# Kernel optimization log

Hardware: AMD Instinct MI355X
Metric: run time of the kernel (lower is better)

## Reference

```python
import jax, jax.numpy as jnp
import numpy as np

ALPHA = 5.0   # surrogate sharpness (cfg.alpha)
C = 0.4       # surrogate scale (cfg.c)
Q = 120.0     # adaptation current scale (cfg.q)
THR = 1.0     # spike threshold

@jax.custom_vjp
def spike(u_thr):
    # Heaviside forward; SLAYER-style surrogate gradient injection backward.
    return (u_thr > 0).astype(u_thr.dtype)

def _spike_fwd(u_thr):
    return spike(u_thr), u_thr

def _spike_bwd(u_thr, g):
    return (g * C * jnp.exp(-ALPHA * jnp.abs(u_thr)),)

spike.defvjp(_spike_fwd, _spike_bwd)


def setup_inputs() -> dict:
    key = jax.random.key(0)
    ks = jax.random.split(key, 8)
    B, T, I, N = 32, 2000, 256, 512
    x = jax.random.normal(ks[0], (B, T, I), dtype=jnp.float32)
    lim = 1.0 / np.sqrt(I)
    weight = jax.random.uniform(ks[1], (N, I), jnp.float32, -lim, lim)
    bias = jnp.zeros((N,), jnp.float32)
    # orthogonal init for recurrent weights (torch.nn.init.orthogonal_)
    g = jax.random.normal(ks[2], (N, N), jnp.float32)
    q_, r_ = jnp.linalg.qr(g)
    recurrent = q_ * jnp.sign(jnp.diagonal(r_))[None, :]
    # membrane / adaptation decays: exp(-dt/tau), tau uniform in cfg ranges
    tau_u = jax.random.uniform(ks[3], (N,), jnp.float32, 5.0, 25.0)
    tau_w = jax.random.uniform(ks[4], (N,), jnp.float32, 60.0, 300.0)
    decay_u = jnp.exp(-1.0 / tau_u)
    decay_w = jnp.exp(-1.0 / tau_w)
    a = jax.random.uniform(ks[5], (N,), jnp.float32, 0.0, 1.0)
    b = jax.random.uniform(ks[6], (N,), jnp.float32, 0.0, 2.0)
    return dict(x=x, weight=weight, bias=bias, recurrent=recurrent,
                decay_u=decay_u, decay_w=decay_w, a=a, b=b)


def reference(x, weight, bias, recurrent, decay_u, decay_w, a, b):
    # soma current for all timesteps at once: [B, T, N]
    cur = jnp.einsum('bti,ni->btn', x, weight) + bias
    B, T, N = cur.shape
    u0 = jnp.zeros((B, N), cur.dtype)  # u0 param is zero-init (train_u0=False)
    z0 = jnp.zeros((B, N), cur.dtype)
    w0 = jnp.zeros((B, N), cur.dtype)

    def step(carry, c_t):
        u_tm1, z_tm1, w_tm1 = carry
        c_t = c_t + z_tm1 @ recurrent.T               # recurrent input
        u = decay_u * u_tm1 + (1.0 - decay_u) * (c_t - w_tm1)
        z = spike(u - THR)
        zd = jax.lax.stop_gradient(z)
        u = u * (1.0 - zd)                            # reset to u_rest = 0
        w = decay_w * w_tm1 + (1.0 - decay_w) * (a * u_tm1 + b * z_tm1) * Q
        return (u, z, w), z

    cur_t = jnp.swapaxes(cur, 0, 1)                   # [T, B, N]
    _, zs = jax.lax.scan(step, (u0, z0, w0), cur_t)
    return jnp.swapaxes(zs, 0, 1)                     # [B, T, N]
```

## Files before the change

kernel.cpp:

```cpp
#include <hip/hip_runtime.h>
#include <cstdint>
#include <cstddef>

#define NB 32
#define NT 2000
#define NI 256
#define NN 512
#define M_TOT (NB * NT)
#define DS 8

typedef float f32x4 __attribute__((ext_vector_type(4)));

__global__ void transpose_R(const float* __restrict__ R, float* __restrict__ Rt) {
    int idx = blockIdx.x * blockDim.x + threadIdx.x;
    if (idx >= NN * NN) return;
    int j = idx >> 9;
    int n = idx & (NN - 1);
    Rt[idx] = R[n * NN + j];
}

#define GBM 128
#define GBN 128
#define GBK 16
__global__ __launch_bounds__(256) void gemm_xw(const float* __restrict__ A,
                                               const float* __restrict__ Wt,
                                               const float* __restrict__ bias,
                                               float* __restrict__ C) {
    __shared__ float As[GBK][GBM];
    __shared__ float Bs[GBK][GBN];
    const int tid = threadIdx.x;
    const int bm = blockIdx.x * GBM;
    const int bn = blockIdx.y * GBN;
    const int tx = tid & 15, ty = tid >> 4;
    const int lrow = tid >> 1;
    const int lk = (tid & 1) * 8;
    float acc[8][8] = {};
    const float* Arow = A + (size_t)(bm + lrow) * NI + lk;
    const float* Brow = Wt + (size_t)(bn + lrow) * NI + lk;
    for (int k0 = 0; k0 < NI; k0 += GBK) {
        float4 a0 = *(const float4*)(Arow + k0);
        float4 a1 = *(const float4*)(Arow + k0 + 4);
        float4 b0 = *(const float4*)(Brow + k0);
        float4 b1 = *(const float4*)(Brow + k0 + 4);
        __syncthreads();
        As[lk + 0][lrow] = a0.x; As[lk + 1][lrow] = a0.y;
        As[lk + 2][lrow] = a0.z; As[lk + 3][lrow] = a0.w;
        As[lk + 4][lrow] = a1.x; As[lk + 5][lrow] = a1.y;
        As[lk + 6][lrow] = a1.z; As[lk + 7][lrow] = a1.w;
        Bs[lk + 0][lrow] = b0.x; Bs[lk + 1][lrow] = b0.y;
        Bs[lk + 2][lrow] = b0.z; Bs[lk + 3][lrow] = b0.w;
        Bs[lk + 4][lrow] = b1.x; Bs[lk + 5][lrow] = b1.y;
        Bs[lk + 6][lrow] = b1.z; Bs[lk + 7][lrow] = b1.w;
        __syncthreads();
        #pragma unroll
        for (int k = 0; k < GBK; ++k) {
            float4 av0 = *(const float4*)&As[k][ty * 8];
            float4 av1 = *(const float4*)&As[k][ty * 8 + 4];
            float4 bv0 = *(const float4*)&Bs[k][tx * 8];
            float4 bv1 = *(const float4*)&Bs[k][tx * 8 + 4];
            float a_[8] = {av0.x, av0.y, av0.z, av0.w, av1.x, av1.y, av1.z, av1.w};
            float b_[8] = {bv0.x, bv0.y, bv0.z, bv0.w, bv1.x, bv1.y, bv1.z, bv1.w};
            #pragma unroll
            for (int i = 0; i < 8; ++i)
                #pragma unroll
                for (int j = 0; j < 8; ++j)
                    acc[i][j] += a_[i] * b_[j];
        }
    }
    #pragma unroll
    for (int i = 0; i < 8; ++i) {
        const int row = bm + ty * 8 + i;
        #pragma unroll
        for (int j = 0; j < 8; ++j) {
            const int col = bn + tx * 8 + j;
            C[(size_t)row * NN + col] = acc[i][j] + bias[col];
        }
    }
}


#define UPD(C_, R_, DU_, ODU_, DW_, ODW_, A_, B_, U_, W_, Z_) do {               \
    float cc_   = __fadd_rn((C_), (R_));                                         \
    float unew_ = __fadd_rn(__fmul_rn((DU_), (U_)),                              \
                            __fmul_rn((ODU_), __fsub_rn(cc_, (W_))));            \
    float zn_   = (__fsub_rn(unew_, 1.0f) > 0.0f) ? 1.0f : 0.0f;                 \
    float s_    = __fadd_rn(__fmul_rn((A_), (U_)), __fmul_rn((B_), (Z_)));       \
    float wnew_ = __fadd_rn(__fmul_rn((DW_), (W_)),                              \
                            __fmul_rn(__fmul_rn((ODW_), s_), 120.0f));           \
    (U_) = __fmul_rn(unew_, __fsub_rn(1.0f, zn_));                               \
    (W_) = wnew_;                                                                \
    (Z_) = zn_;                                                                  \
} while (0)

#define HLOAD(DA, DB, PTR)                                                       \
    asm volatile("global_load_dwordx4 %0, %2, off\n\t"                           \
                 "global_load_dwordx4 %1, %2, off offset:16"                     \
                 : "=&v"(DA), "=&v"(DB) : "v"(PTR))

__global__ __launch_bounds__(128, 1) void scan_pc(const float* __restrict__ cur,
        const float* __restrict__ Rm,
        const float* __restrict__ du_g, const float* __restrict__ dw_g,
        const float* __restrict__ a_g, const float* __restrict__ b_g,
        float* __restrict__ out) {
    __shared__ float curlds[DS][NN];
    const int tid = threadIdx.x;
    const int lane = tid & 63;
    const int b = blockIdx.x;
    const float* curb = cur + (size_t)b * NT * NN;

    if (tid >= 64) {
        const int off = lane << 3;
        float4 q0a, q0b, q1a, q1b, q2a, q2b, q3a, q3b;
        #define PLOAD(QA, QB, STEP) do {                                          \
            const float* p_ = curb + (size_t)(STEP) * NN + off;                   \
            QA = *(const float4*)p_; QB = *(const float4*)(p_ + 4);               \
        } while (0)
        #define PSTORE(QA, QB, STEP) do {                                         \
            int sl_ = (STEP) & (DS - 1);                                          \
            *(float4*)&curlds[sl_][off] = QA;                                     \
            *(float4*)&curlds[sl_][off + 4] = QB;                                 \
        } while (0)
        PLOAD(q0a, q0b, 0); PLOAD(q1a, q1b, 1); PLOAD(q2a, q2b, 2); PLOAD(q3a, q3b, 3);
        PSTORE(q0a, q0b, 0); PSTORE(q1a, q1b, 1); PSTORE(q2a, q2b, 2);
        PLOAD(q0a, q0b, 4); PLOAD(q1a, q1b, 5); PLOAD(q2a, q2b, 6);
        #define PSTEP(QA, QB, T) do {                                             \
            int ws_ = (T) + 3; if (ws_ > NT - 1) ws_ = NT - 1;                    \
            int ls_ = (T) + 7; if (ls_ > NT - 1) ls_ = NT - 1;                    \
            PSTORE(QA, QB, ws_);                                                  \
            PLOAD(QA, QB, ls_);                                                   \
            asm volatile("s_waitcnt lgkmcnt(0)" ::: "memory");                    \
            __builtin_amdgcn_s_barrier();                                         \
        } while (0)
        for (int t = 0; t < NT; t += 4) {
            PSTEP(q3a, q3b, t + 0);
            PSTEP(q0a, q0b, t + 1);
            PSTEP(q1a, q1b, t + 2);
            PSTEP(q2a, q2b, t + 3);
        }
        #undef PSTEP
        #undef PSTORE
        #undef PLOAD
    } else {
        const int n0 = lane << 3;

        const float4 du0 = *(const float4*)(du_g + n0);
        const float4 du1 = *(const float4*)(du_g + n0 + 4);
        const float4 dw0 = *(const float4*)(dw_g + n0);
        const float4 dw1 = *(const float4*)(dw_g + n0 + 4);
        const float4 an0 = *(const float4*)(a_g + n0);
        const float4 an1 = *(const float4*)(a_g + n0 + 4);
        const float4 bn0 = *(const float4*)(b_g + n0);
        const float4 bn1 = *(const float4*)(b_g + n0 + 4);
        const float4 odu0 = {1.0f - du0.x, 1.0f - du0.y, 1.0f - du0.z, 1.0f - du0.w};
        const float4 odu1 = {1.0f - du1.x, 1.0f - du1.y, 1.0f - du1.z, 1.0f - du1.w};
        const float4 odw0 = {1.0f - dw0.x, 1.0f - dw0.y, 1.0f - dw0.z, 1.0f - dw0.w};
        const float4 odw1 = {1.0f - dw1.x, 1.0f - dw1.y, 1.0f - dw1.z, 1.0f - dw1.w};

        float4 u0 = {0,0,0,0}, u1 = {0,0,0,0};
        float4 w0 = {0,0,0,0}, w1 = {0,0,0,0};
        float4 z0 = {0,0,0,0}, z1 = {0,0,0,0};
        unsigned long long m0=0,m1=0,m2=0,m3=0,m4=0,m5=0,m6=0,m7=0;

        float* outp = out + (size_t)b * NT * NN + n0;

        for (int t = 0; t < NT; ++t) {
            __builtin_amdgcn_s_barrier();
            __builtin_amdgcn_sched_barrier(0);
            asm volatile("" ::: "memory");
            const int slot = t & (DS - 1);
            float4 c0 = *(const float4*)&curlds[slot][n0];
            float4 c1 = *(const float4*)&curlds[slot][n0 + 4];

            float4 r0 = {0,0,0,0}, r1 = {0,0,0,0};
            if (m0 | m1 | m2 | m3 | m4 | m5 | m6 | m7) {
                #define HEADJ(MM, E) ((MM) ? ((__builtin_ctzll(MM) << 3) + (E)) : 0)
                const float* hp0 = Rm + ((size_t)HEADJ(m0, 0) << 9) + n0;
                const float* hp1 = Rm + ((size_t)HEADJ(m1, 1) << 9) + n0;
                const float* hp2 = Rm + ((size_t)HEADJ(m2, 2) << 9) + n0;
                const float* hp3 = Rm + ((size_t)HEADJ(m3, 3) << 9) + n0;
                const float* hp4 = Rm + ((size_t)HEADJ(m4, 4) << 9) + n0;
                const float* hp5 = Rm + ((size_t)HEADJ(m5, 5) << 9) + n0;
                const float* hp6 = Rm + ((size_t)HEADJ(m6, 6) << 9) + n0;
                const float* hp7 = Rm + ((size_t)HEADJ(m7, 7) << 9) + n0;
                #undef HEADJ
                f32x4 h0a, h0b, h1a, h1b, h2a, h2b, h3a, h3b;
                f32x4 h4a, h4b, h5a, h5b, h6a, h6b, h7a, h7b;
                HLOAD(h0a, h0b, hp0);
                HLOAD(h1a, h1b, hp1);
                HLOAD(h2a, h2b, hp2);
                HLOAD(h3a, h3b, hp3);
                HLOAD(h4a, h4b, hp4);
                HLOAD(h5a, h5b, hp5);
                HLOAD(h6a, h6b, hp6);
                HLOAD(h7a, h7b, hp7);
                asm volatile("s_waitcnt vmcnt(0)" ::: "memory");
                __builtin_amdgcn_sched_barrier(0);

                #define ACC(QA, QB) do {                                          \
                    r0.x = __fadd_rn(r0.x, (QA).x); r0.y = __fadd_rn(r0.y, (QA).y);\
                    r0.z = __fadd_rn(r0.z, (QA).z); r0.w = __fadd_rn(r0.w, (QA).w);\
                    r1.x = __fadd_rn(r1.x, (QB).x); r1.y = __fadd_rn(r1.y, (QB).y);\
                    r1.z = __fadd_rn(r1.z, (QB).z); r1.w = __fadd_rn(r1.w, (QB).w);\
                } while (0)
                #define PROC(MM, E, HA, HB) do {                                  \
                    if (MM) {                                                     \
                        ACC(HA, HB);                                              \
                        unsigned long long g_ = (MM) & ((MM) - 1);                \
                        while (g_) {                                              \
                            int l_ = __builtin_ctzll(g_); g_ &= g_ - 1;           \
                            int j_ = (l_ << 3) + (E);                             \
                            const float* rp_ = Rm + ((size_t)j_ << 9) + n0;       \
                            float4 q0_ = *(const float4*)rp_;                     \
                            float4 q1_ = *(const float4*)(rp_ + 4);               \
                            ACC(q0_, q1_);                                        \
                        }                                                         \
                    }                                                             \
                } while (0)
                PROC(m0, 0, h0a, h0b); PROC(m1, 1, h1a, h1b);
                PROC(m2, 2, h2a, h2b); PROC(m3, 3, h3a, h3b);
                PROC(m4, 4, h4a, h4b); PROC(m5, 5, h5a, h5b);
                PROC(m6, 6, h6a, h6b); PROC(m7, 7, h7a, h7b);
                #undef PROC
                #undef ACC
            }

            UPD(c0.x, r0.x, du0.x, odu0.x, dw0.x, odw0.x, an0.x, bn0.x, u0.x, w0.x, z0.x);
            UPD(c0.y, r0.y, du0.y, odu0.y, dw0.y, odw0.y, an0.y, bn0.y, u0.y, w0.y, z0.y);
            UPD(c0.z, r0.z, du0.z, odu0.z, dw0.z, odw0.z, an0.z, bn0.z, u0.z, w0.z, z0.z);
            UPD(c0.w, r0.w, du0.w, odu0.w, dw0.w, odw0.w, an0.w, bn0.w, u0.w, w0.w, z0.w);
            UPD(c1.x, r1.x, du1.x, odu1.x, dw1.x, odw1.x, an1.x, bn1.x, u1.x, w1.x, z1.x);
            UPD(c1.y, r1.y, du1.y, odu1.y, dw1.y, odw1.y, an1.y, bn1.y, u1.y, w1.y, z1.y);
            UPD(c1.z, r1.z, du1.z, odu1.z, dw1.z, odw1.z, an1.z, bn1.z, u1.z, w1.z, z1.z);
            UPD(c1.w, r1.w, du1.w, odu1.w, dw1.w, odw1.w, an1.w, bn1.w, u1.w, w1.w, z1.w);

            m0 = __ballot(z0.x > 0.5f);
            m1 = __ballot(z0.y > 0.5f);
            m2 = __ballot(z0.z > 0.5f);
            m3 = __ballot(z0.w > 0.5f);
            m4 = __ballot(z1.x > 0.5f);
            m5 = __ballot(z1.y > 0.5f);
            m6 = __ballot(z1.z > 0.5f);
            m7 = __ballot(z1.w > 0.5f);

            *(float4*)outp = z0;
            *(float4*)(outp + 4) = z1;
            outp += NN;
        }
    }
}

__global__ __launch_bounds__(64) void scan_fallback(const float* __restrict__ cur,
        const float* __restrict__ Rm,
        const float* __restrict__ du_g, const float* __restrict__ dw_g,
        const float* __restrict__ a_g, const float* __restrict__ b_g,
        float* __restrict__ out) {
    const int lane = threadIdx.x & 63;
    const int b = blockIdx.x;
    const int n0 = lane << 3;
    const float4 du0 = *(const float4*)(du_g + n0);
    const float4 du1 = *(const float4*)(du_g + n0 + 4);
    const float4 dw0 = *(const float4*)(dw_g + n0);
    const float4 dw1 = *(const float4*)(dw_g + n0 + 4);
    const float4 an0 = *(const float4*)(a_g + n0);
    const float4 an1 = *(const float4*)(a_g + n0 + 4);
    const float4 bn0 = *(const float4*)(b_g + n0);
    const float4 bn1 = *(const float4*)(b_g + n0 + 4);
    const float4 odu0 = {1.0f - du0.x, 1.0f - du0.y, 1.0f - du0.z, 1.0f - du0.w};
    const float4 odu1 = {1.0f - du1.x, 1.0f - du1.y, 1.0f - du1.z, 1.0f - du1.w};
    const float4 odw0 = {1.0f - dw0.x, 1.0f - dw0.y, 1.0f - dw0.z, 1.0f - dw0.w};
    const float4 odw1 = {1.0f - dw1.x, 1.0f - dw1.y, 1.0f - dw1.z, 1.0f - dw1.w};
    float4 u0 = {0,0,0,0}, u1 = {0,0,0,0};
    float4 w0 = {0,0,0,0}, w1 = {0,0,0,0};
    float4 z0 = {0,0,0,0}, z1 = {0,0,0,0};
    unsigned long long m0=0,m1=0,m2=0,m3=0,m4=0,m5=0,m6=0,m7=0;
    const float* curp = cur + (size_t)b * NT * NN + n0;
    float* outp = out + (size_t)b * NT * NN + n0;
    for (int t = 0; t < NT; ++t) {
        float4 c0 = *(const float4*)(curp);
        float4 c1 = *(const float4*)(curp + 4);
        curp += NN;
        float4 r0 = {0,0,0,0}, r1 = {0,0,0,0};
        #define GATHER(MM, E) do {                                                \
            unsigned long long g_ = (MM);                                         \
            while (g_) {                                                          \
                int l_ = __builtin_ctzll(g_); g_ &= g_ - 1;                       \
                int j_ = (l_ << 3) + (E);                                         \
                float q0x_ = Rm[(size_t)(n0 + 0) * NN + j_];                      \
                float q0y_ = Rm[(size_t)(n0 + 1) * NN + j_];                      \
                float q0z_ = Rm[(size_t)(n0 + 2) * NN + j_];                      \
                float q0w_ = Rm[(size_t)(n0 + 3) * NN + j_];                      \
                float q1x_ = Rm[(size_t)(n0 + 4) * NN + j_];                      \
                float q1y_ = Rm[(size_t)(n0 + 5) * NN + j_];                      \
                float q1z_ = Rm[(size_t)(n0 + 6) * NN + j_];                      \
                float q1w_ = Rm[(size_t)(n0 + 7) * NN + j_];                      \
                r0.x = __fadd_rn(r0.x, q0x_); r0.y = __fadd_rn(r0.y, q0y_);       \
                r0.z = __fadd_rn(r0.z, q0z_); r0.w = __fadd_rn(r0.w, q0w_);       \
                r1.x = __fadd_rn(r1.x, q1x_); r1.y = __fadd_rn(r1.y, q1y_);       \
                r1.z = __fadd_rn(r1.z, q1z_); r1.w = __fadd_rn(r1.w, q1w_);       \
            }                                                                     \
        } while (0)
        GATHER(m0, 0); GATHER(m1, 1); GATHER(m2, 2); GATHER(m3, 3);
        GATHER(m4, 4); GATHER(m5, 5); GATHER(m6, 6); GATHER(m7, 7);
        #undef GATHER
        UPD(c0.x, r0.x, du0.x, odu0.x, dw0.x, odw0.x, an0.x, bn0.x, u0.x, w0.x, z0.x);
        UPD(c0.y, r0.y, du0.y, odu0.y, dw0.y, odw0.y, an0.y, bn0.y, u0.y, w0.y, z0.y);
        UPD(c0.z, r0.z, du0.z, odu0.z, dw0.z, odw0.z, an0.z, bn0.z, u0.z, w0.z, z0.z);
        UPD(c0.w, r0.w, du0.w, odu0.w, dw0.w, odw0.w, an0.w, bn0.w, u0.w, w0.w, z0.w);
        UPD(c1.x, r1.x, du1.x, odu1.x, dw1.x, odw1.x, an1.x, bn1.x, u1.x, w1.x, z1.x);
        UPD(c1.y, r1.y, du1.y, odu1.y, dw1.y, odw1.y, an1.y, bn1.y, u1.y, w1.y, z1.y);
        UPD(c1.z, r1.z, du1.z, odu1.z, dw1.z, odw1.z, an1.z, bn1.z, u1.z, w1.z, z1.z);
        UPD(c1.w, r1.w, du1.w, odu1.w, dw1.w, odw1.w, an1.w, bn1.w, u1.w, w1.w, z1.w);
        m0 = __ballot(z0.x > 0.5f);
        m1 = __ballot(z0.y > 0.5f);
        m2 = __ballot(z0.z > 0.5f);
        m3 = __ballot(z0.w > 0.5f);
        m4 = __ballot(z1.x > 0.5f);
        m5 = __ballot(z1.y > 0.5f);
        m6 = __ballot(z1.z > 0.5f);
        m7 = __ballot(z1.w > 0.5f);
        *(float4*)outp = z0;
        *(float4*)(outp + 4) = z1;
        outp += NN;
    }
}

extern "C" void kernel_launch(void* const* d_in, const int* in_sizes, int n_in,
                              void* d_out, int out_size, void* d_ws, size_t ws_size,
                              hipStream_t stream) {
    const float* x    = (const float*)d_in[0];
    const float* W    = (const float*)d_in[1];
    const float* bias = (const float*)d_in[2];
    const float* R    = (const float*)d_in[3];
    const float* du   = (const float*)d_in[4];
    const float* dw   = (const float*)d_in[5];
    const float* a    = (const float*)d_in[6];
    const float* b    = (const float*)d_in[7];
    float* out = (float*)d_out;

    const size_t curBytes = (size_t)M_TOT * NN * sizeof(float);
    const size_t rtBytes  = (size_t)NN * NN * sizeof(float);
    float* Rt  = nullptr;
    float* cur;
    if (ws_size >= rtBytes + curBytes) {
        Rt  = (float*)d_ws;
        cur = (float*)d_ws + (size_t)NN * NN;
    } else if (ws_size >= rtBytes) {
        Rt  = (float*)d_ws;
        cur = out;
    } else {
        cur = out;
    }

    if (Rt) {
        transpose_R<<<(NN * NN + 255) / 256, 256, 0, stream>>>(R, Rt);
    }
    dim3 ggrid(M_TOT / GBM, NN / GBN);
    gemm_xw<<<ggrid, 256, 0, stream>>>(x, W, bias, cur);
    if (Rt) {
        scan_pc<<<NB, 128, 0, stream>>>(cur, Rt, du, dw, a, b, out);
    } else {
        scan_fallback<<<NB, 64, 0, stream>>>(cur, R, du, dw, a, b, out);
    }
}
```

Baseline: 1.113 ms.

## Prefetch first two spike rows per mask right after ballot, split LDS layout

Moves the head recurrent-row loads from the start of the next step to right after the ballot, so they overlap the output stores and the barrier wait. It also loads the first two spiking rows per mask group instead of one. The LDS cur buffer is re-laid out into two halves of 256 floats with lane<<2 indexing, presumably to reduce bank conflicts on the float4 reads and writes. The cost is 64 extra VGPRs held across the loop, plus inline asm loads that stay outstanding across the barrier until vmcnt(0).

After: 1.230 ms. 10.5% more time.

```diff
diff --git a/kernel.cpp b/kernel.cpp
--- a/kernel.cpp
+++ b/kernel.cpp
@@ -102,7 +102,7 @@
         const float* __restrict__ du_g, const float* __restrict__ dw_g,
         const float* __restrict__ a_g, const float* __restrict__ b_g,
         float* __restrict__ out) {
-    __shared__ float curlds[DS][NN];
+    __shared__ float curlds[DS][2][256];
     const int tid = threadIdx.x;
     const int lane = tid & 63;
     const int b = blockIdx.x;
@@ -110,6 +110,7 @@
 
     if (tid >= 64) {
         const int off = lane << 3;
+        const int lo4 = lane << 2;
         float4 q0a, q0b, q1a, q1b, q2a, q2b, q3a, q3b;
         #define PLOAD(QA, QB, STEP) do {                                          \
             const float* p_ = curb + (size_t)(STEP) * NN + off;                   \
@@ -117,8 +118,8 @@
         } while (0)
         #define PSTORE(QA, QB, STEP) do {                                         \
             int sl_ = (STEP) & (DS - 1);                                          \
-            *(float4*)&curlds[sl_][off] = QA;                                     \
-            *(float4*)&curlds[sl_][off + 4] = QB;                                 \
+            *(float4*)&curlds[sl_][0][lo4] = QA;                                  \
+            *(float4*)&curlds[sl_][1][lo4] = QB;                                  \
         } while (0)
         PLOAD(q0a, q0b, 0); PLOAD(q1a, q1b, 1); PLOAD(q2a, q2b, 2); PLOAD(q3a, q3b, 3);
         PSTORE(q0a, q0b, 0); PSTORE(q1a, q1b, 1); PSTORE(q2a, q2b, 2);
@@ -142,6 +143,7 @@
         #undef PLOAD
     } else {
         const int n0 = lane << 3;
+        const int lo4 = lane << 2;
 
         const float4 du0 = *(const float4*)(du_g + n0);
         const float4 du1 = *(const float4*)(du_g + n0 + 4);
@@ -161,6 +163,9 @@
         float4 z0 = {0,0,0,0}, z1 = {0,0,0,0};
         unsigned long long m0=0,m1=0,m2=0,m3=0,m4=0,m5=0,m6=0,m7=0;
 
+        f32x4 h0a,h0b,h0c,h0d, h1a,h1b,h1c,h1d, h2a,h2b,h2c,h2d, h3a,h3b,h3c,h3d;
+        f32x4 h4a,h4b,h4c,h4d, h5a,h5b,h5c,h5d, h6a,h6b,h6c,h6d, h7a,h7b,h7c,h7d;
+
         float* outp = out + (size_t)b * NT * NN + n0;
 
         for (int t = 0; t < NT; ++t) {
@@ -168,31 +173,11 @@
             __builtin_amdgcn_sched_barrier(0);
             asm volatile("" ::: "memory");
             const int slot = t & (DS - 1);
-            float4 c0 = *(const float4*)&curlds[slot][n0];
-            float4 c1 = *(const float4*)&curlds[slot][n0 + 4];
+            float4 c0 = *(const float4*)&curlds[slot][0][lo4];
+            float4 c1 = *(const float4*)&curlds[slot][1][lo4];
 
             float4 r0 = {0,0,0,0}, r1 = {0,0,0,0};
             if (m0 | m1 | m2 | m3 | m4 | m5 | m6 | m7) {
-                #define HEADJ(MM, E) ((MM) ? ((__builtin_ctzll(MM) << 3) + (E)) : 0)
-                const float* hp0 = Rm + ((size_t)HEADJ(m0, 0) << 9) + n0;
-                const float* hp1 = Rm + ((size_t)HEADJ(m1, 1) << 9) + n0;
-                const float* hp2 = Rm + ((size_t)HEADJ(m2, 2) << 9) + n0;
-                const float* hp3 = Rm + ((size_t)HEADJ(m3, 3) << 9) + n0;
-                const float* hp4 = Rm + ((size_t)HEADJ(m4, 4) << 9) + n0;
-                const float* hp5 = Rm + ((size_t)HEADJ(m5, 5) << 9) + n0;
-                const float* hp6 = Rm + ((size_t)HEADJ(m6, 6) << 9) + n0;
-                const float* hp7 = Rm + ((size_t)HEADJ(m7, 7) << 9) + n0;
-                #undef HEADJ
-                f32x4 h0a, h0b, h1a, h1b, h2a, h2b, h3a, h3b;
-                f32x4 h4a, h4b, h5a, h5b, h6a, h6b, h7a, h7b;
-                HLOAD(h0a, h0b, hp0);
-                HLOAD(h1a, h1b, hp1);
-                HLOAD(h2a, h2b, hp2);
-                HLOAD(h3a, h3b, hp3);
-                HLOAD(h4a, h4b, hp4);
-                HLOAD(h5a, h5b, hp5);
-                HLOAD(h6a, h6b, hp6);
-                HLOAD(h7a, h7b, hp7);
                 asm volatile("s_waitcnt vmcnt(0)" ::: "memory");
                 __builtin_amdgcn_sched_barrier(0);
 
@@ -202,25 +187,33 @@
                     r1.x = __fadd_rn(r1.x, (QB).x); r1.y = __fadd_rn(r1.y, (QB).y);\
                     r1.z = __fadd_rn(r1.z, (QB).z); r1.w = __fadd_rn(r1.w, (QB).w);\
                 } while (0)
-                #define PROC(MM, E, HA, HB) do {                                  \
+                #define PROC2(MM, E, HA, HB, HC, HD) do {                         \
                     if (MM) {                                                     \
                         ACC(HA, HB);                                              \
                         unsigned long long g_ = (MM) & ((MM) - 1);                \
-                        while (g_) {                                              \
-                            int l_ = __builtin_ctzll(g_); g_ &= g_ - 1;           \
-                            int j_ = (l_ << 3) + (E);                             \
-                            const float* rp_ = Rm + ((size_t)j_ << 9) + n0;       \
-                            float4 q0_ = *(const float4*)rp_;                     \
-                            float4 q1_ = *(const float4*)(rp_ + 4);               \
-                            ACC(q0_, q1_);                                        \
+                        if (g_) {                                                 \
+                            ACC(HC, HD);                                          \
+                            g_ &= g_ - 1;                                         \
+                            while (g_) {     \
+                                int l_ = __builtin_ctzll(g_); g_ &= g_ - 1;       \
+                                int j_ = (l_ << 3) + (E);                         \
+                                const float* rp_ = Rm + ((size_t)j_ << 9) + n0;   \
+                                float4 q0_ = *(const float4*)rp_;                 \
+                                float4 q1_ = *(const float4*)(rp_ + 4);           \
+                                ACC(q0_, q1_);                                    \
+                            }                                                     \
                         }                                                         \
                     }                                                             \
                 } while (0)
-                PROC(m0, 0, h0a, h0b); PROC(m1, 1, h1a, h1b);
-                PROC(m2, 2, h2a, h2b); PROC(m3, 3, h3a, h3b);
-                PROC(m4, 4, h4a, h4b); PROC(m5, 5, h5a, h5b);
-                PROC(m6, 6, h6a, h6b); PROC(m7, 7, h7a, h7b);
-                #undef PROC
+                PROC2(m0, 0, h0a, h0b, h0c, h0d);
+                PROC2(m1, 1, h1a, h1b, h1c, h1d);
+                PROC2(m2, 2, h2a, h2b, h2c, h2d);
+                PROC2(m3, 3, h3a, h3b, h3c, h3d);
+                PROC2(m4, 4, h4a, h4b, h4c, h4d);
+                PROC2(m5, 5, h5a, h5b, h5c, h5d);
+                PROC2(m6, 6, h6a, h6b, h6c, h6d);
+                PROC2(m7, 7, h7a, h7b, h7c, h7d);
+                #undef PROC2
                 #undef ACC
             }
 
@@ -241,6 +234,29 @@
             m5 = __ballot(z1.y > 0.5f);
             m6 = __ballot(z1.z > 0.5f);
             m7 = __ballot(z1.w > 0.5f);
+
+            if (m0 | m1 | m2 | m3 | m4 | m5 | m6 | m7) {
+                #define ISSUE2(MM, E, HA, HB, HC, HD) do {                        \
+                    unsigned long long g1_ = (MM);                                \
+                    unsigned long long g2_ = g1_ ? (g1_ & (g1_ - 1)) : 0ULL;      \
+                    int ja_ = g1_ ? ((__builtin_ctzll(g1_) << 3) + (E)) : 0;      \
+                    int jb_ = g2_ ? ((__builtin_ctzll(g2_) << 3) + (E)) : 0;      \
+                    const float* pa_ = Rm + ((size_t)ja_ << 9) + n0;              \
+                    const float* pb_ = Rm + ((size_t)jb_ << 9) + n0;              \
+                    HLOAD(HA, HB, pa_);                                           \
+                    HLOAD(HC, HD, pb_);                                           \
+                } while (0)
+                ISSUE2(m0, 0, h0a, h0b, h0c, h0d);
+                ISSUE2(m1, 1, h1a, h1b, h1c, h1d);
+                ISSUE2(m2, 2, h2a, h2b, h2c, h2d);
+                ISSUE2(m3, 3, h3a, h3b, h3c, h3d);
+                ISSUE2(m4, 4, h4a, h4b, h4c, h4d);
+                ISSUE2(m5, 5, h5a, h5b, h5c, h5d);
+                ISSUE2(m6, 6, h6a, h6b, h6c, h6d);
+                ISSUE2(m7, 7, h7a, h7b, h7c, h7d);
+                #undef ISSUE2
+                __builtin_amdgcn_sched_barrier(0);
+            }
 
             *(float4*)outp = z0;
             *(float4*)(outp + 4) = z1;
```
